# Kernel optimization log

Hardware: AMD Instinct MI355X
Metric: run time of the kernel (lower is better)

Reference implementation:

```python
import jax, jax.numpy as jnp
import numpy as np

HEADS = 4
DIM_HEAD = 128


def setup_inputs() -> dict:
    key = jax.random.key(0)
    k1, k2, k3 = jax.random.split(key, 3)
    dim = 256
    hidden = HEADS * DIM_HEAD  # 512
    x = jax.random.normal(k1, (16, dim, 64, 64), dtype=jnp.float32)
    # 1x1 conv weights stored as [out_ch, in_ch] (kernel dims squeezed)
    w_qkv = jax.random.normal(k2, (hidden * 3, dim), dtype=jnp.float32) * (1.0 / np.sqrt(dim))
    w_out = jax.random.normal(k3, (dim, hidden), dtype=jnp.float32) * (1.0 / np.sqrt(hidden))
    b_out = jnp.zeros((dim,), dtype=jnp.float32)
    return {"x": x, "w_qkv": w_qkv, "w_out": w_out, "b_out": b_out}


def reference(x, w_qkv, w_out, b_out):
    b, c, h, w = x.shape
    n = h * w
    # 1x1 conv == per-pixel linear projection
    qkv = jnp.einsum('bchw,oc->bohw', x, w_qkv)           # [b, 3*heads*dh, h, w]
    qkv = qkv.reshape(b, 3, HEADS, DIM_HEAD, n)           # 'b (qkv heads c) h w -> qkv b heads c (h w)'
    q, k, v = qkv[:, 0], qkv[:, 1], qkv[:, 2]             # [b, heads, dh, n]
    k = jax.nn.softmax(k, axis=-1)                        # softmax over spatial positions
    context = jnp.einsum('bhdn,bhen->bhde', k, v)         # [b, heads, dh, dh]
    out = jnp.einsum('bhde,bhdn->bhen', context, q)       # [b, heads, dh, n]
    out = out.reshape(b, HEADS * DIM_HEAD, h, w)          # 'b heads c (h w) -> b (heads c) h w'
    y = jnp.einsum('bchw,oc->bohw', out, w_out) + b_out[None, :, None, None]
    return y
```

## Files before the change

### kernel.cpp

```cpp
#include <hip/hip_runtime.h>

#define BATCH 16
#define CIN   256
#define NSP   4096
#define HID   512

typedef short v8s __attribute__((ext_vector_type(8)));
typedef float v4f __attribute__((ext_vector_type(4)));

__device__ __forceinline__ unsigned short f2bf(float f) {
    union { float f; unsigned u; } a; a.f = f;
    unsigned r = a.u + 0x7fffu + ((a.u >> 16) & 1u);
    return (unsigned short)(r >> 16);
}

__device__ __forceinline__ void gld_lds16(const unsigned short* g, unsigned short* l) {
    __builtin_amdgcn_global_load_lds(
        (const __attribute__((address_space(1))) unsigned int*)g,
        (__attribute__((address_space(3))) unsigned int*)l,
        16, 0, 0);
}


__global__ __launch_bounds__(256) void k_prep(const float* __restrict__ x,
                                              const float* __restrict__ wq,
                                              unsigned short* __restrict__ xbf,
                                              unsigned short* __restrict__ xT,
                                              unsigned short* __restrict__ wbf,
                                              unsigned short* __restrict__ wqT,
                                              float* __restrict__ zacc) {
    const int bid = blockIdx.x;
    const int t = threadIdx.x;
    if (bid >= 4320) {
        zacc[(bid - 4320) * 256 + t] = 0.f;
        return;
    }
    if (bid >= 4096) {
        const int wid = bid - 4096;
        if (wid < 192) {
            const int g = wid * 256 + t;
            const float4 f0 = *(const float4*)(wq + (size_t)g * 8);
            const float4 f1 = *(const float4*)(wq + (size_t)g * 8 + 4);
            union { unsigned short s[8]; uint4 u; } p;
            p.s[0] = f2bf(f0.x); p.s[1] = f2bf(f0.y); p.s[2] = f2bf(f0.z); p.s[3] = f2bf(f0.w);
            p.s[4] = f2bf(f1.x); p.s[5] = f2bf(f1.y); p.s[6] = f2bf(f1.z); p.s[7] = f2bf(f1.w);
            *(uint4*)(wbf + (size_t)g * 8) = p.u;
            return;
        }
        __shared__ float tile[64 * 65];
        const int bb = wid - 192;
        const int u0 = (bb & 7) * 64, c0 = (bb >> 3) * 64;
        {
            const int cl = (t & 15) * 4, ul = t >> 4;
            #pragma unroll
            for (int i = 0; i < 4; i++) {
                int u = ul + i * 16;
                const float4 f = *(const float4*)(wq + (size_t)(u0 + u) * CIN + c0 + cl);
                *(float4*)(&tile[u * 65 + cl]) = f;
            }
        }
        __syncthreads();
        {
            const int ul4 = (t & 15) * 4, cl = t >> 4;
            #pragma unroll
            for (int i = 0; i < 4; i++) {
                int c = cl + i * 16;
                union { unsigned short s[4]; uint2 u; } p;
                #pragma unroll
                for (int j = 0; j < 4; j++)
                    p.s[j] = f2bf(tile[(ul4 + j) * 65 + c]);
                *(uint2*)(wqT + (size_t)(c0 + c) * HID + u0 + ul4) = p.u;
            }
        }
        return;
    }
    __shared__ float tile[64 * 65];
    const int n0 = (bid & 63) * 64, c0 = ((bid >> 6) & 3) * 64, bz = bid >> 8;
    const float* xb = x + (size_t)bz * CIN * NSP;
    {
        const int nl = (t & 15) * 4, cl = t >> 4;
        #pragma unroll
        for (int i = 0; i < 4; i++) {
            int c = cl + i * 16;
            const float4 f = *(const float4*)(xb + (size_t)(c0 + c) * NSP + n0 + nl);
            *(float4*)(&tile[c * 65 + nl]) = f;
            union { unsigned short s[4]; uint2 u; } p;
            p.s[0] = f2bf(f.x); p.s[1] = f2bf(f.y); p.s[2] = f2bf(f.z); p.s[3] = f2bf(f.w);
            *(uint2*)(xbf + ((size_t)bz * CIN + c0 + c) * NSP + n0 + nl) = p.u;
        }
    }
    __syncthreads();
    {
        const int cl4 = (t & 15) * 4, nl = t >> 4;
        #pragma unroll
        for (int i = 0; i < 4; i++) {
            int n = nl + i * 16;
            union { unsigned short s[4]; uint2 u; } p;
            #pragma unroll
            for (int j = 0; j < 4; j++)
                p.s[j] = f2bf(tile[(cl4 + j) * 65 + n]);
            *(uint2*)(xT + ((size_t)bz * NSP + n0 + n) * CIN + c0 + cl4) = p.u;
        }
    }
}

__global__ __launch_bounds__(256) void k_k(const unsigned short* __restrict__ wbf,
                                           const unsigned short* __restrict__ xT,
                                           unsigned short* __restrict__ expk,
                                           float* __restrict__ zacc) {
    __shared__ __align__(16) unsigned short As[128 * 64];
    __shared__ __align__(16) unsigned short Bs[128 * 64];
    const int t = threadIdx.x;
    const int id = blockIdx.x;
    const int bz = id >> 7;
    const int r7 = id & 127;
    const int xcd = r7 & 7, s7 = r7 >> 3;
    const int bn = (xcd << 2) | (s7 & 3);
    const int bm = s7 >> 2;
    const int d0 = bm * 128, n0 = bn * 128;
    const int lane = t & 63, wv = t >> 6;
    const int quad = lane >> 4, l15 = lane & 15;
    const int wmN = (wv & 1) * 64, wnD = (wv >> 1) * 64;

    const int srow8 = lane >> 3, sslot = lane & 7;
    const int scol = ((sslot - srow8) & 7) * 8;
    const int sw0 = ((quad + l15) & 7) * 8;

    const unsigned short* Ag = xT + ((size_t)bz * NSP + n0 + wv * 32 + srow8) * CIN + scol;
    const unsigned short* Bg = wbf + (size_t)(512 + d0 + wv * 32 + srow8) * CIN + scol;
    unsigned short* Al = As + wv * 32 * 64;
    unsigned short* Bl = Bs + wv * 32 * 64;

    v4f acc[4][4];
    #pragma unroll
    for (int i = 0; i < 4; i++)
        #pragma unroll
        for (int j = 0; j < 4; j++) acc[i][j] = (v4f)0.f;

    for (int kk = 0; kk < CIN; kk += 64) {
        #pragma unroll
        for (int cc = 0; cc < 4; cc++) {
            gld_lds16(Ag + (size_t)(cc * 8) * CIN + kk, Al + cc * 8 * 64);
            gld_lds16(Bg + (size_t)(cc * 8) * CIN + kk, Bl + cc * 8 * 64);
        }
        __syncthreads();
        #pragma unroll
        for (int h = 0; h < 2; h++) {
            const int sw = sw0 ^ (h * 32);
            v8s af[4], bfr[4];
            #pragma unroll
            for (int mi = 0; mi < 4; mi++) {
                union { v8s v; uint4 u; } rr;
                rr.u = *(const uint4*)(&As[(wmN + mi * 16 + l15) * 64 + sw]);
                af[mi] = rr.v;
            }
            #pragma unroll
            for (int ni = 0; ni < 4; ni++) {
                union { v8s v; uint4 u; } rr;
                rr.u = *(const uint4*)(&Bs[(wnD + ni * 16 + l15) * 64 + sw]);
                bfr[ni] = rr.v;
            }
            #pragma unroll
            for (int mi = 0; mi < 4; mi++)
                #pragma unroll
                for (int ni = 0; ni < 4; ni++)
                    acc[mi][ni] = __builtin_amdgcn_mfma_f32_16x16x32_bf16(af[mi], bfr[ni], acc[mi][ni], 0, 0, 0);
        }
        __syncthreads();
    }

    float za[4] = {0.f, 0.f, 0.f, 0.f};
    #pragma unroll
    for (int ni = 0; ni < 4; ni++) {
        const int d = d0 + wnD + ni * 16 + l15;
        #pragma unroll
        for (int mi = 0; mi < 4; mi++) {
            const int nb = n0 + wmN + mi * 16 + quad * 4;
            union { unsigned short s[4]; uint2 u; } p;
            #pragma unroll
            for (int rr = 0; rr < 4; rr++) {
                float e = __expf(acc[mi][ni][rr]);
                za[ni] += e;
                p.s[rr] = f2bf(e);
            }
            *(uint2*)(expk + ((size_t)bz * 512 + d) * NSP + nb) = p.u;
        }
    }
    #pragma unroll
    for (int ni = 0; ni < 4; ni++) {
        float z = za[ni];
        z += __shfl_xor(z, 16);
        z += __shfl_xor(z, 32);
        if (quad == 0)
            atomicAdd(&zacc[bz * 512 + d0 + wnD + ni * 16 + l15], z);
    }
}

__global__ __launch_bounds__(256) void k_S(const unsigned short* __restrict__ expk,
                                           const unsigned short* __restrict__ xbf,
                                           float* __restrict__ Sp) {
    __shared__ __align__(16) unsigned short As[128 * 64];
    __shared__ __align__(16) unsigned short Bs[128 * 64];
    const int t = threadIdx.x;
    const int id = blockIdx.x;
    const int hc = id >> 6;
    const int h = hc >> 1, ch = hc & 1;
    const int bkc = id & 63;
    const int b = bkc >> 2, kc = bkc & 3;
    const int kw = kc * 1024;
    const int lane = t & 63, wv = t >> 6, quad = lane >> 4, l15 = lane & 15;
    const int wmC = (wv & 1) * 64, wnD = (wv >> 1) * 64;

    const int srow8 = lane >> 3, sslot = lane & 7;
    const int scol = ((sslot - srow8) & 7) * 8;
    const int sw0 = ((quad + l15) & 7) * 8;

    const unsigned short* Ag = xbf + ((size_t)b * CIN + ch * 128 + wv * 32 + srow8) * NSP + kw + scol;
    const unsigned short* Bg = expk + ((size_t)b * 512 + h * 128 + wv * 32 + srow8) * NSP + kw + scol;
    unsigned short* Al = As + wv * 32 * 64;
    unsigned short* Bl = Bs + wv * 32 * 64;

    v4f acc[4][4];
    #pragma unroll
    for (int i = 0; i < 4; i++)
        #pragma unroll
        for (int j = 0; j < 4; j++) acc[i][j] = (v4f)0.f;

    for (int kk = 0; kk < 1024; kk += 64) {
        #pragma unroll
        for (int cc = 0; cc < 4; cc++) {
            gld_lds16(Ag + (size_t)(cc * 8) * NSP + kk, Al + cc * 8 * 64);
            gld_lds16(Bg + (size_t)(cc * 8) * NSP + kk, Bl + cc * 8 * 64);
        }
        __syncthreads();
        #pragma unroll
        for (int h2 = 0; h2 < 2; h2++) {
            const int sw = sw0 ^ (h2 * 32);
            v8s af[4], bfr[4];
            #pragma unroll
            for (int mi = 0; mi < 4; mi++) {
                union { v8s v; uint4 u; } rr;
                rr.u = *(const uint4*)(&As[(wmC + mi * 16 + l15) * 64 + sw]);
                af[mi] = rr.v;
            }
            #pragma unroll
            for (int ni = 0; ni < 4; ni++) {
                union { v8s v; uint4 u; } rr;
                rr.u = *(const uint4*)(&Bs[(wnD + ni * 16 + l15) * 64 + sw]);
                bfr[ni] = rr.v;
            }
            #pragma unroll
            for (int mi = 0; mi < 4; mi++)
                #pragma unroll
                for (int ni = 0; ni < 4; ni++)
                    acc[mi][ni] = __builtin_amdgcn_mfma_f32_16x16x32_bf16(af[mi], bfr[ni], acc[mi][ni], 0, 0, 0);
        }
        __syncthreads();
    }

    const int bh = b * 4 + h;
    float* outp = Sp + ((size_t)(bh * 2 + ch) * 4 + kc) * 16384;
    #pragma unroll
    for (int ni = 0; ni < 4; ni++) {
        const int d = wnD + ni * 16 + l15;
        #pragma unroll
        for (int mi = 0; mi < 4; mi++) {
            const int c = wmC + mi * 16 + quad * 4;
            *(v4f*)(outp + d * 128 + c) = acc[mi][ni];
        }
    }
}

__global__ __launch_bounds__(256) void k_sred(const float* __restrict__ Sp,
                                              unsigned short* __restrict__ Sred) {
    const int qv = blockIdx.x * 256 + threadIdx.x;
    const int bh = qv >> 13, r = qv & 8191;
    const int dl = r >> 6, cq6 = r & 63;
    const int ch = cq6 >> 5, clq = cq6 & 31;
    const float* p = Sp + ((size_t)(bh * 2 + ch) * 4) * 16384 + dl * 128 + clq * 4;
    float4 s = *(const float4*)p;
    #pragma unroll
    for (int kc = 1; kc < 4; kc++) {
        const float4 f = *(const float4*)(p + (size_t)kc * 16384);
        s.x += f.x; s.y += f.y; s.z += f.z; s.w += f.w;
    }
    union { unsigned short us[4]; uint2 u; } pk;
    pk.us[0] = f2bf(s.x); pk.us[1] = f2bf(s.y); pk.us[2] = f2bf(s.z); pk.us[3] = f2bf(s.w);
    *(uint2*)(Sred + (size_t)bh * 32768 + dl * 256 + cq6 * 4) = pk.u;
}

__global__ __launch_bounds__(256) void k_redwc(const unsigned short* __restrict__ Sred,
                                               const float* __restrict__ zacc,
                                               const unsigned short* __restrict__ wbf,
                                               const float* __restrict__ w_out,
                                               unsigned short* __restrict__ Wc) {
    __shared__ unsigned short Ds[128 * 136];
    __shared__ float zinv[128];
    const int t = threadIdx.x;
    const int bh = blockIdx.x;  const int b = bh >> 2, h = bh & 3;
    const int lane = t & 63, wv = t >> 6, quad = lane >> 4, l15 = lane & 15;

    if (t < 128) zinv[t] = 1.0f / zacc[b * 512 + h * 128 + t];
    __syncthreads();

    {
        const int wm = (wv & 1) * 64, wn = (wv >> 1) * 64;
        const unsigned short* Sb = Sred + (size_t)bh * 32768;
        const unsigned short* Vb = wbf + (size_t)(1024 + h * 128) * CIN;
        v4f acc[4][4];
        #pragma unroll
        for (int i = 0; i < 4; i++)
            #pragma unroll
            for (int j = 0; j < 4; j++) acc[i][j] = (v4f)0.f;
        for (int kk = 0; kk < CIN; kk += 32) {
            v8s af[4], bfr[4];
            #pragma unroll
            for (int mi = 0; mi < 4; mi++) {
                union { v8s v; uint4 u; } rr;
                rr.u = *(const uint4*)(Sb + (size_t)(wm + mi * 16 + l15) * 256 + kk + quad * 8);
                af[mi] = rr.v;
            }
            #pragma unroll
            for (int ni = 0; ni < 4; ni++) {
                union { v8s v; uint4 u; } rr;
                rr.u = *(const uint4*)(Vb + (size_t)(wn + ni * 16 + l15) * 256 + kk + quad * 8);
                bfr[ni] = rr.v;
            }
            #pragma unroll
            for (int mi = 0; mi < 4; mi++)
                #pragma unroll
                for (int ni = 0; ni < 4; ni++)
                    acc[mi][ni] = __builtin_amdgcn_mfma_f32_16x16x32_bf16(af[mi], bfr[ni], acc[mi][ni], 0, 0, 0);
        }
        float zq[4][4];
        #pragma unroll
        for (int mi = 0; mi < 4; mi++)
            #pragma unroll
            for (int rr = 0; rr < 4; rr++)
                zq[mi][rr] = zinv[wm + mi * 16 + quad * 4 + rr];
        #pragma unroll
        for (int mi = 0; mi < 4; mi++)
            #pragma unroll
            for (int ni = 0; ni < 4; ni++)
                #pragma unroll
                for (int rr = 0; rr < 4; rr++)
                    Ds[(wm + mi * 16 + quad * 4 + rr) * 136 + wn + ni * 16 + l15] =
                        f2bf(acc[mi][ni][rr] * zq[mi][rr]);
    }
    __syncthreads();

    {
        const int wm = wv * 64;
        v4f acc[4][8];
        #pragma unroll
        for (int i = 0; i < 4; i++)
            #pragma unroll
            for (int j = 0; j < 8; j++) acc[i][j] = (v4f)0.f;
        for (int kk = 0; kk < 128; kk += 32) {
            v8s af[4], bfr[8];
            #pragma unroll
            for (int mi = 0; mi < 4; mi++) {
                int o = wm + mi * 16 + l15;
                const float* wp = w_out + (size_t)o * HID + h * 128 + kk + quad * 8;
                float4 f0 = *(const float4*)wp;
                float4 f1 = *(const float4*)(wp + 4);
                union { v8s v; unsigned short s[8]; } r;
                r.s[0] = f2bf(f0.x); r.s[1] = f2bf(f0.y); r.s[2] = f2bf(f0.z); r.s[3] = f2bf(f0.w);
                r.s[4] = f2bf(f1.x); r.s[5] = f2bf(f1.y); r.s[6] = f2bf(f1.z); r.s[7] = f2bf(f1.w);
                af[mi] = r.v;
            }
            #pragma unroll
            for (int ni = 0; ni < 8; ni++) {
                union { v8s v; uint4 u; } r;
                r.u = *(const uint4*)(&Ds[(ni * 16 + l15) * 136 + kk + quad * 8]);
                bfr[ni] = r.v;
            }
            #pragma unroll
            for (int mi = 0; mi < 4; mi++)
                #pragma unroll
                for (int ni = 0; ni < 8; ni++)
                    acc[mi][ni] = __builtin_amdgcn_mfma_f32_16x16x32_bf16(af[mi], bfr[ni], acc[mi][ni], 0, 0, 0);
        }
        #pragma unroll
        for (int ni = 0; ni < 8; ni++) {
            int d = ni * 16 + l15;
            #pragma unroll
            for (int mi = 0; mi < 4; mi++)
                #pragma unroll
                for (int rr = 0; rr < 4; rr++) {
                    int o = wm + mi * 16 + quad * 4 + rr;
                    Wc[((size_t)b * 256 + o) * HID + h * 128 + d] = f2bf(acc[mi][ni][rr]);
                }
        }
    }
}

__global__ __launch_bounds__(256) void k_chain(const unsigned short* __restrict__ Wc,
                                               const unsigned short* __restrict__ wqT,
                                               unsigned short* __restrict__ Weff) {
    __shared__ __align__(16) unsigned short As[128 * 64];
    __shared__ __align__(16) unsigned short Bs[128 * 64];
    const int t = threadIdx.x;
    const int c0 = blockIdx.x * 128, o0 = blockIdx.y * 128, bz = blockIdx.z;
    const int lane = t & 63, wv = t >> 6, quad = lane >> 4, l15 = lane & 15;
    const int wmC = (wv & 1) * 64, wnO = (wv >> 1) * 64;

    const int srow8 = lane >> 3, sslot = lane & 7;
    const int scol = ((sslot - srow8) & 7) * 8;
    const int sw0 = ((quad + l15) & 7) * 8;

    const unsigned short* Ag = wqT + (size_t)(c0 + wv * 32 + srow8) * HID + scol;
    const unsigned short* Bg = Wc + ((size_t)bz * 256 + o0 + wv * 32 + srow8) * HID + scol;
    unsigned short* Al = As + wv * 32 * 64;
    unsigned short* Bl = Bs + wv * 32 * 64;

    v4f acc[4][4];
    #pragma unroll
    for (int i = 0; i < 4; i++)
        #pragma unroll
        for (int j = 0; j < 4; j++) acc[i][j] = (v4f)0.f;

    for (int kk = 0; kk < HID; kk += 64) {
        #pragma unroll
        for (int cc = 0; cc < 4; cc++) {
            gld_lds16(Ag + (size_t)(cc * 8) * HID + kk, Al + cc * 8 * 64);
            gld_lds16(Bg + (size_t)(cc * 8) * HID + kk, Bl + cc * 8 * 64);
        }
        __syncthreads();
        #pragma unroll
        for (int h = 0; h < 2; h++) {
            const int sw = sw0 ^ (h * 32);
            v8s af[4], bfr[4];
            #pragma unroll
            for (int mi = 0; mi < 4; mi++) {
                union { v8s v; uint4 u; } rr;
                rr.u = *(const uint4*)(&As[(wmC + mi * 16 + l15) * 64 + sw]);
                af[mi] = rr.v;
            }
            #pragma unroll
            for (int ni = 0; ni < 4; ni++) {
                union { v8s v; uint4 u; } rr;
                rr.u = *(const uint4*)(&Bs[(wnO + ni * 16 + l15) * 64 + sw]);
                bfr[ni] = rr.v;
            }
            #pragma unroll
            for (int mi = 0; mi < 4; mi++)
                #pragma unroll
                for (int ni = 0; ni < 4; ni++)
                    acc[mi][ni] = __builtin_amdgcn_mfma_f32_16x16x32_bf16(af[mi], bfr[ni], acc[mi][ni], 0, 0, 0);
        }
        __syncthreads();
    }
    #pragma unroll
    for (int ni = 0; ni < 4; ni++) {
        const int o = o0 + wnO + ni * 16 + l15;
        #pragma unroll
        for (int mi = 0; mi < 4; mi++) {
            const int c = c0 + wmC + mi * 16 + quad * 4;
            union { unsigned short s[4]; uint2 u; } p;
            #pragma unroll
            for (int rr = 0; rr < 4; rr++) p.s[rr] = f2bf(acc[mi][ni][rr]);
            *(uint2*)(Weff + ((size_t)bz * 256 + o) * 256 + c) = p.u;
        }
    }
}

__global__ __launch_bounds__(256) void k_y(const unsigned short* __restrict__ Weff,
                                           const unsigned short* __restrict__ xT,
                                           const float* __restrict__ b_out,
                                           float* __restrict__ y) {
    __shared__ __align__(16) unsigned short As[128 * 64];
    __shared__ __align__(16) unsigned short Bs[128 * 64];
    const int t = threadIdx.x;
    const int o0 = blockIdx.x * 128;
    const int n0 = blockIdx.y * 128;
    const int bz = blockIdx.z;
    const int lane = t & 63, wv = t >> 6, quad = lane >> 4, l15 = lane & 15;
    const int wmN = (wv & 1) * 64, wnO = (wv >> 1) * 64;

    const int srow8 = lane >> 3, sslot = lane & 7;
    const int scol = ((sslot - srow8) & 7) * 8;
    const int sw0 = ((quad + l15) & 7) * 8;

    const unsigned short* Ag = xT + ((size_t)bz * NSP + n0 + wv * 32 + srow8) * CIN + scol;
    const unsigned short* Bg = Weff + ((size_t)bz * 256 + o0 + wv * 32 + srow8) * CIN + scol;
    unsigned short* Al = As + wv * 32 * 64;
    unsigned short* Bl = Bs + wv * 32 * 64;

    v4f acc[4][4];
    #pragma unroll
    for (int i = 0; i < 4; i++)
        #pragma unroll
        for (int j = 0; j < 4; j++) acc[i][j] = (v4f)0.f;

    for (int kk = 0; kk < CIN; kk += 64) {
        #pragma unroll
        for (int cc = 0; cc < 4; cc++) {
            gld_lds16(Ag + (size_t)(cc * 8) * CIN + kk, Al + cc * 8 * 64);
            gld_lds16(Bg + (size_t)(cc * 8) * CIN + kk, Bl + cc * 8 * 64);
        }
        __syncthreads();
        #pragma unroll
        for (int h = 0; h < 2; h++) {
            const int sw = sw0 ^ (h * 32);
            v8s af[4], bfr[4];
            #pragma unroll
            for (int mi = 0; mi < 4; mi++) {
                union { v8s v; uint4 u; } rr;
                rr.u = *(const uint4*)(&As[(wmN + mi * 16 + l15) * 64 + sw]);
                af[mi] = rr.v;
            }
            #pragma unroll
            for (int ni = 0; ni < 4; ni++) {
                union { v8s v; uint4 u; } rr;
                rr.u = *(const uint4*)(&Bs[(wnO + ni * 16 + l15) * 64 + sw]);
                bfr[ni] = rr.v;
            }
            #pragma unroll
            for (int mi = 0; mi < 4; mi++)
                #pragma unroll
                for (int ni = 0; ni < 4; ni++)
                    acc[mi][ni] = __builtin_amdgcn_mfma_f32_16x16x32_bf16(af[mi], bfr[ni], acc[mi][ni], 0, 0, 0);
        }
        __syncthreads();
    }
    #pragma unroll
    for (int ni = 0; ni < 4; ni++) {
        const int o = o0 + wnO + ni * 16 + l15;
        const float bias = b_out[o];
        #pragma unroll
        for (int mi = 0; mi < 4; mi++) {
            const int n = n0 + wmN + mi * 16 + quad * 4;
            v4f v = acc[mi][ni];
            v[0] += bias; v[1] += bias; v[2] += bias; v[3] += bias;
            *(v4f*)(y + ((size_t)bz * 256 + o) * NSP + n) = v;
        }
    }
}

extern "C" void kernel_launch(void* const* d_in, const int* in_sizes, int n_in,
                              void* d_out, int out_size, void* d_ws, size_t ws_size,
                              hipStream_t stream) {
    (void)in_sizes; (void)n_in; (void)out_size; (void)ws_size;
    const float* x     = (const float*)d_in[0];
    const float* w_qkv = (const float*)d_in[1];
    const float* w_out = (const float*)d_in[2];
    const float* b_out = (const float*)d_in[3];
    float* y = (float*)d_out;
    char* ws = (char*)d_ws;

    unsigned short* xT   = (unsigned short*)(ws);
    unsigned short* xbf  = (unsigned short*)(ws + 33554432);
    unsigned short* expk = (unsigned short*)(ws + 67108864);
    float*          Sp   = (float*)(ws + 134217728);
    float*          zacc = (float*)(ws + 167772160);
    unsigned short* Sred = (unsigned short*)(ws + 167804928);
    unsigned short* Wc   = (unsigned short*)(ws + 171999232);
    unsigned short* Weff = (unsigned short*)(ws + 176193536);
    unsigned short* wbf  = (unsigned short*)(ws + 178290688);
    unsigned short* wqT  = (unsigned short*)(ws + 179077120);

    k_prep <<<dim3(4352),       256, 0, stream>>>(x, w_qkv, xbf, xT, wbf, wqT, zacc);
    k_k    <<<dim3(2048),       256, 0, stream>>>(wbf, xT, expk, zacc);
    k_S    <<<dim3(512),        256, 0, stream>>>(expk, xbf, Sp);
    k_sred <<<dim3(2048),       256, 0, stream>>>(Sp, Sred);
    k_redwc<<<dim3(64),         256, 0, stream>>>(Sred, zacc, wbf, w_out, Wc);
    k_chain<<<dim3(2, 2, 16),   256, 0, stream>>>(Wc, wqT, Weff);
    k_y    <<<dim3(2, 32, 16),  256, 0, stream>>>(Weff, xT, b_out, y);
}
```

Measured before the change: 245.5 us.

## Fuse key projection, exp, and context GEMM into one kernel

Merges the k projection plus exp kernel and the context GEMM into a single kernel. Each block keeps its 128-row W_k slice in registers, computes exp(K) for a 128-column spatial tile into LDS, and immediately multiplies it against the matching x tile to accumulate the context. This removes the 64 MB bf16 expk round-trip to global memory and one kernel launch. In exchange, the grid shrinks to 256 blocks of 512 threads with large LDS use and heavy register pressure, which may leave compute units underused.

```diff
diff --git a/kernel.cpp b/kernel.cpp
--- a/kernel.cpp
+++ b/kernel.cpp
@@ -104,169 +104,180 @@
     }
 }
 
-__global__ __launch_bounds__(256) void k_k(const unsigned short* __restrict__ wbf,
-                                           const unsigned short* __restrict__ xT,
-                                           unsigned short* __restrict__ expk,
-                                           float* __restrict__ zacc) {
-    __shared__ __align__(16) unsigned short As[128 * 64];
-    __shared__ __align__(16) unsigned short Bs[128 * 64];
+__global__ __launch_bounds__(512, 2) void k_ks(const unsigned short* __restrict__ wbf,
+                                               const unsigned short* __restrict__ xT,
+                                               const unsigned short* __restrict__ xbf,
+                                               float* __restrict__ Sp,
+                                               float* __restrict__ zacc) {
+    __shared__ __align__(16) unsigned short A1s[2][2][128][64];
+    __shared__ __align__(16) unsigned short A2s[2][256][64];
+    __shared__ __align__(16) unsigned short Es[128 * 128];
+
     const int t = threadIdx.x;
     const int id = blockIdx.x;
-    const int bz = id >> 7;
-    const int r7 = id & 127;
-    const int xcd = r7 & 7, s7 = r7 >> 3;
-    const int bn = (xcd << 2) | (s7 & 3);
-    const int bm = s7 >> 2;
-    const int d0 = bm * 128, n0 = bn * 128;
-    const int lane = t & 63, wv = t >> 6;
-    const int quad = lane >> 4, l15 = lane & 15;
-    const int wmN = (wv & 1) * 64, wnD = (wv >> 1) * 64;
-
+    const int bz = id & 15, dblk = (id >> 4) & 3, nc = id >> 6;
+    const int d0 = dblk * 128;
+    const int nbase = nc * 1024;
+    const int lane = t & 63, wv = t >> 6, quad = lane >> 4, l15 = lane & 15;
     const int srow8 = lane >> 3, sslot = lane & 7;
     const int scol = ((sslot - srow8) & 7) * 8;
     const int sw0 = ((quad + l15) & 7) * 8;
-
-    const unsigned short* Ag = xT + ((size_t)bz * NSP + n0 + wv * 32 + srow8) * CIN + scol;
-    const unsigned short* Bg = wbf + (size_t)(512 + d0 + wv * 32 + srow8) * CIN + scol;
-    unsigned short* Al = As + wv * 32 * 64;
-    unsigned short* Bl = Bs + wv * 32 * 64;
-
-    v4f acc[4][4];
+    const int wn = wv & 1, wd1 = wv >> 1;
+    const int wc = wv & 3, wd2 = wv >> 2;
+
+    auto STAGE_A1 = [&](int half, int nrow0) {
+        #pragma unroll
+        for (int i = 0; i < 4; i++) {
+            const int flat = wv * 4 + i;
+            const int kl = flat >> 4, rb = flat & 15;
+            gld_lds16(xT + ((size_t)bz * NSP + nrow0 + rb * 8 + srow8) * CIN + (half * 2 + kl) * 64 + scol,
+                      &A1s[half][kl][rb * 8][0]);
+        }
+    };
+    auto STAGE_A2 = [&](int n0s) {
+        #pragma unroll
+        for (int i = 0; i < 8; i++) {
+            const int flat = wv * 8 + i;
+            const int kst = flat >> 5, rb = flat & 31;
+            gld_lds16(xbf + ((size_t)bz * CIN + rb * 8 + srow8) * NSP + n0s + kst * 64 + scol,
+                      &A2s[kst][rb * 8][0]);
+        }
+    };
+
+    {
+        #pragma unroll
+        for (int i = 0; i < 8; i++) {
+            const int flat = wv * 8 + i;
+            const int kk = flat >> 4, rb = flat & 15;
+            gld_lds16(wbf + (size_t)(512 + d0 + rb * 8 + srow8) * CIN + kk * 64 + scol,
+                      &A2s[0][0][0] + (kk * 128 + rb * 8) * 64);
+        }
+    }
+    __syncthreads();
+    v8s Wkf[4][2][2];
+    #pragma unroll
+    for (int kk = 0; kk < 4; kk++)
+        #pragma unroll
+        for (int ni = 0; ni < 2; ni++)
+            #pragma unroll
+            for (int h = 0; h < 2; h++) {
+                union { v8s v; uint4 u; } rr;
+                rr.u = *(const uint4*)(&A2s[0][0][0] +
+                        (size_t)(kk * 128 + wd1 * 32 + ni * 16 + l15) * 64 + (sw0 ^ (h * 32)));
+                Wkf[kk][ni][h] = rr.v;
+            }
+    __syncthreads();
+
+    v4f acc2[4][4];
     #pragma unroll
     for (int i = 0; i < 4; i++)
         #pragma unroll
-        for (int j = 0; j < 4; j++) acc[i][j] = (v4f)0.f;
-
-    for (int kk = 0; kk < CIN; kk += 64) {
-        #pragma unroll
-        for (int cc = 0; cc < 4; cc++) {
-            gld_lds16(Ag + (size_t)(cc * 8) * CIN + kk, Al + cc * 8 * 64);
-            gld_lds16(Bg + (size_t)(cc * 8) * CIN + kk, Bl + cc * 8 * 64);
-        }
-        __syncthreads();
-        #pragma unroll
-        for (int h = 0; h < 2; h++) {
-            const int sw = sw0 ^ (h * 32);
-            v8s af[4], bfr[4];
+        for (int j = 0; j < 4; j++) acc2[i][j] = (v4f)0.f;
+    float za[2] = {0.f, 0.f};
+
+    STAGE_A1(0, nbase);
+    STAGE_A1(1, nbase);
+
+    for (int nt = 0; nt < 8; nt++) {
+        const int n0s = nbase + nt * 128;
+        __syncthreads();
+        STAGE_A2(n0s);
+
+        v4f acc1[4][2];
+        #pragma unroll
+        for (int i = 0; i < 4; i++)
+            #pragma unroll
+            for (int j = 0; j < 2; j++) acc1[i][j] = (v4f)0.f;
+
+        __builtin_amdgcn_s_setprio(1);
+        #pragma unroll
+        for (int kk = 0; kk < 4; kk++) {
+            #pragma unroll
+            for (int h = 0; h < 2; h++) {
+                v8s af[4];
+                #pragma unroll
+                for (int mi = 0; mi < 4; mi++) {
+                    union { v8s v; uint4 u; } rr;
+                    rr.u = *(const uint4*)(&A1s[kk >> 1][kk & 1][wn * 64 + mi * 16 + l15][0] + (sw0 ^ (h * 32)));
+                    af[mi] = rr.v;
+                }
+                #pragma unroll
+                for (int mi = 0; mi < 4; mi++)
+                    #pragma unroll
+                    for (int ni = 0; ni < 2; ni++)
+                        acc1[mi][ni] = __builtin_amdgcn_mfma_f32_16x16x32_bf16(af[mi], Wkf[kk][ni][h], acc1[mi][ni], 0, 0, 0);
+            }
+        }
+        __builtin_amdgcn_s_setprio(0);
+
+        #pragma unroll
+        for (int ni = 0; ni < 2; ni++) {
+            const int d = wd1 * 32 + ni * 16 + l15;
             #pragma unroll
             for (int mi = 0; mi < 4; mi++) {
-                union { v8s v; uint4 u; } rr;
-                rr.u = *(const uint4*)(&As[(wmN + mi * 16 + l15) * 64 + sw]);
-                af[mi] = rr.v;
-            }
-            #pragma unroll
-            for (int ni = 0; ni < 4; ni++) {
-                union { v8s v; uint4 u; } rr;
-                rr.u = *(const uint4*)(&Bs[(wnD + ni * 16 + l15) * 64 + sw]);
-                bfr[ni] = rr.v;
-            }
-            #pragma unroll
-            for (int mi = 0; mi < 4; mi++)
-                #pragma unroll
-                for (int ni = 0; ni < 4; ni++)
-                    acc[mi][ni] = __builtin_amdgcn_mfma_f32_16x16x32_bf16(af[mi], bfr[ni], acc[mi][ni], 0, 0, 0);
-        }
-        __syncthreads();
-    }
-
-    float za[4] = {0.f, 0.f, 0.f, 0.f};
-    #pragma unroll
-    for (int ni = 0; ni < 4; ni++) {
-        const int d = d0 + wnD + ni * 16 + l15;
-        #pragma unroll
-        for (int mi = 0; mi < 4; mi++) {
-            const int nb = n0 + wmN + mi * 16 + quad * 4;
-            union { unsigned short s[4]; uint2 u; } p;
-            #pragma unroll
-            for (int rr = 0; rr < 4; rr++) {
-                float e = __expf(acc[mi][ni][rr]);
-                za[ni] += e;
-                p.s[rr] = f2bf(e);
-            }
-            *(uint2*)(expk + ((size_t)bz * 512 + d) * NSP + nb) = p.u;
-        }
-    }
-    #pragma unroll
-    for (int ni = 0; ni < 4; ni++) {
+                union { unsigned short s[4]; uint2 u; } p;
+                #pragma unroll
+                for (int rr = 0; rr < 4; rr++) {
+                    float e = __expf(acc1[mi][ni][rr]);
+                    za[ni] += e;
+                    p.s[rr] = f2bf(e);
+                }
+                const int slot = (mi * 2 + (quad >> 1) + d) & 7;
+                *(uint2*)(&Es[d * 128 + wn * 64 + slot * 8 + (quad & 1) * 4]) = p.u;
+            }
+        }
+        __syncthreads();
+        if (nt < 7) {
+            STAGE_A1(0, n0s + 128);
+            STAGE_A1(1, n0s + 128);
+        }
+
+        __builtin_amdgcn_s_setprio(1);
+        #pragma unroll
+        for (int kst = 0; kst < 2; kst++) {
+            #pragma unroll
+            for (int h = 0; h < 2; h++) {
+                v8s af[4], bfr[4];
+                #pragma unroll
+                for (int mi = 0; mi < 4; mi++) {
+                    union { v8s v; uint4 u; } rr;
+                    rr.u = *(const uint4*)(&A2s[kst][wc * 64 + mi * 16 + l15][0] + (sw0 ^ (h * 32)));
+                    af[mi] = rr.v;
+                }
+                #pragma unroll
+                for (int ni = 0; ni < 4; ni++) {
+                    union { v8s v; uint4 u; } rr;
+                    rr.u = *(const uint4*)(&Es[(wd2 * 64 + ni * 16 + l15) * 128 + kst * 64 + (sw0 ^ (h * 32))]);
+                    bfr[ni] = rr.v;
+                }
+                #pragma unroll
+                for (int mi = 0; mi < 4; mi++)
+                    #pragma unroll
+                    for (int ni = 0; ni < 4; ni++)
+                        acc2[mi][ni] = __builtin_amdgcn_mfma_f32_16x16x32_bf16(af[mi], bfr[ni], acc2[mi][ni], 0, 0, 0);
+            }
+        }
+        __builtin_amdgcn_s_setprio(0);
+    }
+
+    #pragma unroll
+    for (int ni = 0; ni < 2; ni++) {
         float z = za[ni];
         z += __shfl_xor(z, 16);
         z += __shfl_xor(z, 32);
         if (quad == 0)
-            atomicAdd(&zacc[bz * 512 + d0 + wnD + ni * 16 + l15], z);
-    }
-}
-
-__global__ __launch_bounds__(256) void k_S(const unsigned short* __restrict__ expk,
-                                           const unsigned short* __restrict__ xbf,
-                                           float* __restrict__ Sp) {
-    __shared__ __align__(16) unsigned short As[128 * 64];
-    __shared__ __align__(16) unsigned short Bs[128 * 64];
-    const int t = threadIdx.x;
-    const int id = blockIdx.x;
-    const int hc = id >> 6;
-    const int h = hc >> 1, ch = hc & 1;
-    const int bkc = id & 63;
-    const int b = bkc >> 2, kc = bkc & 3;
-    const int kw = kc * 1024;
-    const int lane = t & 63, wv = t >> 6, quad = lane >> 4, l15 = lane & 15;
-    const int wmC = (wv & 1) * 64, wnD = (wv >> 1) * 64;
-
-    const int srow8 = lane >> 3, sslot = lane & 7;
-    const int scol = ((sslot - srow8) & 7) * 8;
-    const int sw0 = ((quad + l15) & 7) * 8;
-
-    const unsigned short* Ag = xbf + ((size_t)b * CIN + ch * 128 + wv * 32 + srow8) * NSP + kw + scol;
-    const unsigned short* Bg = expk + ((size_t)b * 512 + h * 128 + wv * 32 + srow8) * NSP + kw + scol;
-    unsigned short* Al = As + wv * 32 * 64;
-    unsigned short* Bl = Bs + wv * 32 * 64;
-
-    v4f acc[4][4];
-    #pragma unroll
-    for (int i = 0; i < 4; i++)
-        #pragma unroll
-        for (int j = 0; j < 4; j++) acc[i][j] = (v4f)0.f;
-
-    for (int kk = 0; kk < 1024; kk += 64) {
-        #pragma unroll
-        for (int cc = 0; cc < 4; cc++) {
-            gld_lds16(Ag + (size_t)(cc * 8) * NSP + kk, Al + cc * 8 * 64);
-            gld_lds16(Bg + (size_t)(cc * 8) * NSP + kk, Bl + cc * 8 * 64);
-        }
-        __syncthreads();
-        #pragma unroll
-        for (int h2 = 0; h2 < 2; h2++) {
-            const int sw = sw0 ^ (h2 * 32);
-            v8s af[4], bfr[4];
-            #pragma unroll
-            for (int mi = 0; mi < 4; mi++) {
-                union { v8s v; uint4 u; } rr;
-                rr.u = *(const uint4*)(&As[(wmC + mi * 16 + l15) * 64 + sw]);
-                af[mi] = rr.v;
-            }
-            #pragma unroll
-            for (int ni = 0; ni < 4; ni++) {
-                union { v8s v; uint4 u; } rr;
-                rr.u = *(const uint4*)(&Bs[(wnD + ni * 16 + l15) * 64 + sw]);
-                bfr[ni] = rr.v;
-            }
-            #pragma unroll
-            for (int mi = 0; mi < 4; mi++)
-                #pragma unroll
-                for (int ni = 0; ni < 4; ni++)
-                    acc[mi][ni] = __builtin_amdgcn_mfma_f32_16x16x32_bf16(af[mi], bfr[ni], acc[mi][ni], 0, 0, 0);
-        }
-        __syncthreads();
-    }
-
-    const int bh = b * 4 + h;
-    float* outp = Sp + ((size_t)(bh * 2 + ch) * 4 + kc) * 16384;
+            atomicAdd(&zacc[bz * 512 + d0 + wd1 * 32 + ni * 16 + l15], z);
+    }
+
+    const int ch = wc >> 1;
+    float* outp = Sp + ((size_t)((bz * 4 + dblk) * 2 + ch) * 4 + nc) * 16384;
     #pragma unroll
     for (int ni = 0; ni < 4; ni++) {
-        const int d = wnD + ni * 16 + l15;
+        const int dl = wd2 * 64 + ni * 16 + l15;
         #pragma unroll
         for (int mi = 0; mi < 4; mi++) {
-            const int c = wmC + mi * 16 + quad * 4;
-            *(v4f*)(outp + d * 128 + c) = acc[mi][ni];
+            const int cl = (wc & 1) * 64 + mi * 16 + quad * 4;
+            *(v4f*)(outp + dl * 128 + cl) = acc2[mi][ni];
         }
     }
 }
@@ -551,7 +562,6 @@
 
     unsigned short* xT   = (unsigned short*)(ws);
     unsigned short* xbf  = (unsigned short*)(ws + 33554432);
-    unsigned short* expk = (unsigned short*)(ws + 67108864);
     float*          Sp   = (float*)(ws + 134217728);
     float*          zacc = (float*)(ws + 167772160);
     unsigned short* Sred = (unsigned short*)(ws + 167804928);
@@ -561,8 +571,7 @@
     unsigned short* wqT  = (unsigned short*)(ws + 179077120);
 
     k_prep <<<dim3(4352),       256, 0, stream>>>(x, w_qkv, xbf, xT, wbf, wqT, zacc);
-    k_k    <<<dim3(2048),       256, 0, stream>>>(wbf, xT, expk, zacc);
-    k_S    <<<dim3(512),        256, 0, stream>>>(expk, xbf, Sp);
+    k_ks   <<<dim3(256),        512, 0, stream>>>(wbf, xT, xbf, Sp, zacc);
     k_sred <<<dim3(2048),       256, 0, stream>>>(Sp, Sred);
     k_redwc<<<dim3(64),         256, 0, stream>>>(Sred, zacc, wbf, w_out, Wc);
     k_chain<<<dim3(2, 2, 16),   256, 0, stream>>>(Wc, wqT, Weff);
```

New measurement: 230.7 us. -6.0%, faster.
